# Performance work log

Hardware: AMD Instinct MI355X
Metric: run time of the kernel (lower is better)

Reference implementation:

```python
import jax, jax.numpy as jnp
import numpy as np

KH, KW = 3, 3      # kernel_size
SH, SW = 1, 1      # stride
MINVAL, MAXVAL = -0.45, -0.15


def setup_inputs() -> dict:
    key = jax.random.key(0)
    kx, kw = jax.random.split(key)
    x = jax.random.normal(kx, (16, 128, 128, 16), dtype=jnp.float32)  # NHWC
    W = jax.random.uniform(kw, (KH, KW, 16, 32), minval=MINVAL, maxval=MAXVAL,
                           dtype=jnp.float32)  # [kh, kw, C_in, filters]
    return {"x": x, "W": W}


def _dilation(x, W):
    # Max-plus sliding-window 'convolution' (VALID padding):
    # out[b,i,j,f] = max_{di,dj,c} x[b, i*SH+di, j*SW+dj, c] + W[di,dj,c,f]
    kh, kw, C, F = W.shape
    B, H, Wd, _ = x.shape
    Hout = (H - kh) // SH + 1
    Wout = (Wd - kw) // SW + 1
    out = jnp.full((B, Hout, Wout, F), -jnp.inf, dtype=x.dtype)
    for di in range(kh):          # small fixed loop over kernel offsets
        for dj in range(kw):
            xs = x[:, di:di + Hout * SH:SH, dj:dj + Wout * SW:SW, :]  # [B,Hout,Wout,C]
            # add W for this offset, reduce max over input channels
            out = jnp.maximum(out, jnp.max(xs[..., :, None] + W[di, dj], axis=3))
    return out


def reference(x, W):
    # erosion(x) = -dilation(-x)
    return -_dilation(-x, W)
```

## Files before the change

kernel.cpp:

```cpp
#include <hip/hip_runtime.h>
#include <math.h>


#define TI 42
#define TROWS (TI + 2)
#define LROW 64

typedef _Float16 h2 __attribute__((ext_vector_type(2)));

__device__ __forceinline__ h2 hmin2(h2 a, h2 b) {
    return __builtin_elementwise_min(a, b);
}

__device__ __forceinline__ h2 pkrtz(float a, float b) {
    auto r = __builtin_amdgcn_cvt_pkrtz(a, b);
    return *reinterpret_cast<h2*>(&r);
}

__device__ __forceinline__ h2 rowmin(const h2* hx, const h2 w[3][4]) {
    h2 t[12];
#pragma unroll
    for (int dj = 0; dj < 3; ++dj)
#pragma unroll
        for (int q = 0; q < 4; ++q)
            t[dj * 4 + q] = hx[dj * 4 + q] - w[dj][q];
#pragma unroll
    for (int k = 0; k < 6; ++k) t[k] = hmin2(t[k], t[k + 6]);
    t[0] = hmin2(t[0], t[3]);
    t[1] = hmin2(t[1], t[4]);
    t[2] = hmin2(t[2], t[5]);
    return hmin2(hmin2(t[0], t[1]), t[2]);
}

__global__ __launch_bounds__(256) void erosion_kernel(
    const float* __restrict__ x, const float* __restrict__ Wt,
    float* __restrict__ out)
{
    __shared__ _Float16 lds[2 * TROWS * LROW];

    const int tid = threadIdx.x;
    const int f  = tid & 31;
    const int ch = (tid >> 5) & 1;
    const int jt = tid >> 6;
    const int b  = blockIdx.z;
    const int i0 = blockIdx.y * TI;
    const int jb = blockIdx.x * 4;
    const int j  = jb + jt;
    const bool writer = (j < 126) && (ch == 0);

    {
        const float* xg = x + (size_t)b * (128 * 128 * 16);
        for (int t = tid; t < TROWS * 12; t += 256) {
            int r   = t / 12;
            int k   = t % 12;
            int cc  = k >> 1;
            int ch2 = k & 1;
            int col = min(jb + cc, 127);
            const float* src = xg + ((size_t)(i0 + r) * 128 + col) * 16 + ch2 * 8;
            float4 lo = *reinterpret_cast<const float4*>(src);
            float4 hi = *reinterpret_cast<const float4*>(src + 4);
            h2 o[4] = { pkrtz(lo.x, lo.y), pkrtz(lo.z, lo.w),
                        pkrtz(hi.x, hi.y), pkrtz(hi.z, hi.w) };
            *reinterpret_cast<float4*>(
                &lds[ch2 * (TROWS * LROW) + r * LROW + cc * 8]) =
                *reinterpret_cast<float4*>(o);
        }
    }

    h2 wh[3][3][4];
#pragma unroll
    for (int di = 0; di < 3; ++di)
#pragma unroll
        for (int dj = 0; dj < 3; ++dj)
#pragma unroll
            for (int q = 0; q < 4; ++q) {
                int p = di * 3 + dj;
                float a = Wt[(p * 16 + ch * 8 + 2 * q) * 32 + f];
                float c = Wt[(p * 16 + ch * 8 + 2 * q + 1) * 32 + f];
                wh[di][dj][q] = pkrtz(a, c);
            }

    __syncthreads();

    const _Float16* lb = &lds[ch * (TROWS * LROW) + jt * 8];
    float* op = out + (((size_t)b * 126 + i0) * 126 + j) * 32 + f;

    const _Float16 HINF = (_Float16)__builtin_huge_valf();
    h2 accB = {HINF, HINF};
    h2 accC = {HINF, HINF};

    auto body = [&](int r, bool do_store) {
        h2 hx[12];
#pragma unroll
        for (int dj = 0; dj < 3; ++dj) {
            float4 raw = *reinterpret_cast<const float4*>(lb + r * LROW + dj * 8);
            const h2* p = reinterpret_cast<const h2*>(&raw);
            hx[dj * 4 + 0] = p[0];
            hx[dj * 4 + 1] = p[1];
            hx[dj * 4 + 2] = p[2];
            hx[dj * 4 + 3] = p[3];
        }

        h2 n0 = rowmin(hx, wh[0]);
        h2 n1 = rowmin(hx, wh[1]);
        h2 n2 = rowmin(hx, wh[2]);

        h2 fin2 = hmin2(accC, n2);
        accC = hmin2(accB, n1);
        accB = n0;

        if (do_store) {
            _Float16 vm = fin2[0] < fin2[1] ? fin2[0] : fin2[1];
            float v = (float)vm;
            v = fminf(v, __shfl_xor(v, 32));
            if (writer)
                op[(size_t)(r - 2) * (126 * 32)] = v;
        }
    };

    body(0, false);
    body(1, false);
#pragma unroll 3
    for (int r = 2; r < TROWS; ++r)
        body(r, true);
}

extern "C" void kernel_launch(void* const* d_in, const int* in_sizes, int n_in,
                              void* d_out, int out_size, void* d_ws, size_t ws_size,
                              hipStream_t stream) {
    const float* x  = (const float*)d_in[0];
    const float* Wt = (const float*)d_in[1];
    float* out = (float*)d_out;

    dim3 grid(32, 3, 16);
    dim3 block(256);
    erosion_kernel<<<grid, block, 0, stream>>>(x, Wt, out);
}
```

Before: 113.6 us.

## Give each thread all 16 input channels and drop the cross-lane shuffle

The channel split across two half-waves goes away. Each thread now reduces over all 16 channels with 72 packed weights held in registers, so the __shfl_xor combine is no longer needed. The block covers 8 output columns instead of 4, the row tile shrinks from 42 to 21, and the grid changes to 16x6x16 while the block count stays the same. LDS becomes a single interleaved buffer with 16 channels per column. In exchange, register pressure roughly doubles for weights and inputs, and the halo row overhead grows because of the shorter row tiles.

```diff
diff --git a/kernel.cpp b/kernel.cpp
--- a/kernel.cpp
+++ b/kernel.cpp
@@ -2,9 +2,10 @@
 #include <math.h>
 
 
-#define TI 42
+#define TI 21
 #define TROWS (TI + 2)
-#define LROW 64
+#define TCOLS 10
+#define CROW (TCOLS * 16)
 
 typedef _Float16 h2 __attribute__((ext_vector_type(2)));
 
@@ -17,72 +18,53 @@
     return *reinterpret_cast<h2*>(&r);
 }
 
-__device__ __forceinline__ h2 rowmin(const h2* hx, const h2 w[3][4]) {
-    h2 t[12];
-#pragma unroll
-    for (int dj = 0; dj < 3; ++dj)
-#pragma unroll
-        for (int q = 0; q < 4; ++q)
-            t[dj * 4 + q] = hx[dj * 4 + q] - w[dj][q];
-#pragma unroll
-    for (int k = 0; k < 6; ++k) t[k] = hmin2(t[k], t[k + 6]);
-    t[0] = hmin2(t[0], t[3]);
-    t[1] = hmin2(t[1], t[4]);
-    t[2] = hmin2(t[2], t[5]);
-    return hmin2(hmin2(t[0], t[1]), t[2]);
-}
-
 __global__ __launch_bounds__(256) void erosion_kernel(
     const float* __restrict__ x, const float* __restrict__ Wt,
     float* __restrict__ out)
 {
-    __shared__ _Float16 lds[2 * TROWS * LROW];
+    __shared__ _Float16 lds[TROWS * CROW];
 
     const int tid = threadIdx.x;
     const int f  = tid & 31;
-    const int ch = (tid >> 5) & 1;
-    const int jt = tid >> 6;
+    const int jt = tid >> 5;
     const int b  = blockIdx.z;
     const int i0 = blockIdx.y * TI;
-    const int jb = blockIdx.x * 4;
+    const int jb = blockIdx.x * 8;
     const int j  = jb + jt;
-    const bool writer = (j < 126) && (ch == 0);
+    const bool writer = (j < 126);
 
     {
         const float* xg = x + (size_t)b * (128 * 128 * 16);
-        for (int t = tid; t < TROWS * 12; t += 256) {
-            int r   = t / 12;
-            int k   = t % 12;
-            int cc  = k >> 1;
-            int ch2 = k & 1;
+        for (int t = tid; t < TROWS * 40; t += 256) {
+            int r   = t / 40;
+            int k   = t % 40;
+            int cc  = k >> 2;
+            int q4  = k & 3;
             int col = min(jb + cc, 127);
-            const float* src = xg + ((size_t)(i0 + r) * 128 + col) * 16 + ch2 * 8;
-            float4 lo = *reinterpret_cast<const float4*>(src);
-            float4 hi = *reinterpret_cast<const float4*>(src + 4);
-            h2 o[4] = { pkrtz(lo.x, lo.y), pkrtz(lo.z, lo.w),
-                        pkrtz(hi.x, hi.y), pkrtz(hi.z, hi.w) };
-            *reinterpret_cast<float4*>(
-                &lds[ch2 * (TROWS * LROW) + r * LROW + cc * 8]) =
-                *reinterpret_cast<float4*>(o);
+            const float* src = xg + ((size_t)(i0 + r) * 128 + col) * 16 + q4 * 4;
+            float4 v = *reinterpret_cast<const float4*>(src);
+            h2 o[2] = { pkrtz(v.x, v.y), pkrtz(v.z, v.w) };
+            *reinterpret_cast<double*>(&lds[r * CROW + cc * 16 + q4 * 4]) =
+                *reinterpret_cast<double*>(o);
         }
     }
 
-    h2 wh[3][3][4];
+    h2 wh[3][3][8];
 #pragma unroll
     for (int di = 0; di < 3; ++di)
 #pragma unroll
         for (int dj = 0; dj < 3; ++dj)
 #pragma unroll
-            for (int q = 0; q < 4; ++q) {
+            for (int q = 0; q < 8; ++q) {
                 int p = di * 3 + dj;
-                float a = Wt[(p * 16 + ch * 8 + 2 * q) * 32 + f];
-                float c = Wt[(p * 16 + ch * 8 + 2 * q + 1) * 32 + f];
+                float a = Wt[(p * 16 + 2 * q) * 32 + f];
+                float c = Wt[(p * 16 + 2 * q + 1) * 32 + f];
                 wh[di][dj][q] = pkrtz(a, c);
             }
 
     __syncthreads();
 
-    const _Float16* lb = &lds[ch * (TROWS * LROW) + jt * 8];
+    const _Float16* lb = &lds[jt * 16];
     float* op = out + (((size_t)b * 126 + i0) * 126 + j) * 32 + f;
 
     const _Float16 HINF = (_Float16)__builtin_huge_valf();
@@ -90,31 +72,44 @@
     h2 accC = {HINF, HINF};
 
     auto body = [&](int r, bool do_store) {
-        h2 hx[12];
+        h2 hx[3][8];
 #pragma unroll
         for (int dj = 0; dj < 3; ++dj) {
-            float4 raw = *reinterpret_cast<const float4*>(lb + r * LROW + dj * 8);
-            const h2* p = reinterpret_cast<const h2*>(&raw);
-            hx[dj * 4 + 0] = p[0];
-            hx[dj * 4 + 1] = p[1];
-            hx[dj * 4 + 2] = p[2];
-            hx[dj * 4 + 3] = p[3];
+            float4 lo = *reinterpret_cast<const float4*>(lb + r * CROW + dj * 16);
+            float4 hi = *reinterpret_cast<const float4*>(lb + r * CROW + dj * 16 + 8);
+            const h2* pl = reinterpret_cast<const h2*>(&lo);
+            const h2* ph = reinterpret_cast<const h2*>(&hi);
+#pragma unroll
+            for (int q = 0; q < 4; ++q) { hx[dj][q] = pl[q]; hx[dj][4 + q] = ph[q]; }
         }
 
-        h2 n0 = rowmin(hx, wh[0]);
-        h2 n1 = rowmin(hx, wh[1]);
-        h2 n2 = rowmin(hx, wh[2]);
+        h2 n[3];
+#pragma unroll
+        for (int di = 0; di < 3; ++di) {
+            h2 t[24];
+#pragma unroll
+            for (int dj = 0; dj < 3; ++dj)
+#pragma unroll
+                for (int q = 0; q < 8; ++q)
+                    t[dj * 8 + q] = hx[dj][q] - wh[di][dj][q];
+#pragma unroll
+            for (int k = 0; k < 12; ++k) t[k] = hmin2(t[k], t[k + 12]);
+#pragma unroll
+            for (int k = 0; k < 6; ++k)  t[k] = hmin2(t[k], t[k + 6]);
+#pragma unroll
+            for (int k = 0; k < 3; ++k)  t[k] = hmin2(t[k], t[k + 3]);
+            n[di] = hmin2(hmin2(t[0], t[1]), t[2]);
+        }
 
-        h2 fin2 = hmin2(accC, n2);
-        accC = hmin2(accB, n1);
-        accB = n0;
+        h2 fin2 = hmin2(accC, n[2]);
+        accC = hmin2(accB, n[1]);
+        accB = n[0];
 
         if (do_store) {
-            _Float16 vm = fin2[0] < fin2[1] ? fin2[0] : fin2[1];
-            float v = (float)vm;
-            v = fminf(v, __shfl_xor(v, 32));
+            _Float16 a = fin2[0], c = fin2[1];
+            _Float16 vm = a < c ? a : c;
             if (writer)
-                op[(size_t)(r - 2) * (126 * 32)] = v;
+                op[(size_t)(r - 2) * (126 * 32)] = (float)vm;
         }
     };
 
@@ -132,7 +127,7 @@
     const float* Wt = (const float*)d_in[1];
     float* out = (float*)d_out;
 
-    dim3 grid(32, 3, 16);
+    dim3 grid(16, 6, 16);
     dim3 block(256);
     erosion_kernel<<<grid, block, 0, stream>>>(x, Wt, out);
 }
```

Measured after the change: 137.6 us. 1.21x slower.

## Halve row tile, stage results in LDS, and prefetch next row into registers

Applied to the files above, without the earlier changes.

Each block now covers half as many output rows, and the grid doubles in the row dimension so more blocks are in flight. Per-row results are no longer reduced with a cross-lane shuffle and written straight to global memory. Each thread instead writes its half-channel minimum to a shared buffer, and after a barrier the block does one pass that combines the two channel halves and stores to global memory. The compute loop also loads the next input row from LDS into registers while the current row is being processed. The extra shared buffer (~13 KB) and the second barrier may reduce occupancy, and halving the tile increases the halo reload overhead.

```diff
diff --git a/kernel.cpp b/kernel.cpp
--- a/kernel.cpp
+++ b/kernel.cpp
@@ -2,9 +2,10 @@
 #include <math.h>
 
 
-#define TI 42
+#define TI 21
 #define TROWS (TI + 2)
 #define LROW 64
+#define VMS 26
 
 typedef _Float16 h2 __attribute__((ext_vector_type(2)));
 
@@ -36,7 +37,8 @@
     const float* __restrict__ x, const float* __restrict__ Wt,
     float* __restrict__ out)
 {
-    __shared__ _Float16 lds[2 * TROWS * LROW];
+    __shared__ _Float16 tile[2 * TROWS * LROW];
+    __shared__ _Float16 vmbuf[256 * VMS];
 
     const int tid = threadIdx.x;
     const int f  = tid & 31;
@@ -45,25 +47,27 @@
     const int b  = blockIdx.z;
     const int i0 = blockIdx.y * TI;
     const int jb = blockIdx.x * 4;
-    const int j  = jb + jt;
-    const bool writer = (j < 126) && (ch == 0);
 
     {
         const float* xg = x + (size_t)b * (128 * 128 * 16);
-        for (int t = tid; t < TROWS * 12; t += 256) {
-            int r   = t / 12;
-            int k   = t % 12;
-            int cc  = k >> 1;
-            int ch2 = k & 1;
-            int col = min(jb + cc, 127);
-            const float* src = xg + ((size_t)(i0 + r) * 128 + col) * 16 + ch2 * 8;
-            float4 lo = *reinterpret_cast<const float4*>(src);
-            float4 hi = *reinterpret_cast<const float4*>(src + 4);
-            h2 o[4] = { pkrtz(lo.x, lo.y), pkrtz(lo.z, lo.w),
-                        pkrtz(hi.x, hi.y), pkrtz(hi.z, hi.w) };
-            *reinterpret_cast<float4*>(
-                &lds[ch2 * (TROWS * LROW) + r * LROW + cc * 8]) =
-                *reinterpret_cast<float4*>(o);
+#pragma unroll
+        for (int pass = 0; pass < 2; ++pass) {
+            int t = tid + pass * 256;
+            if (t < TROWS * 12) {
+                int r   = t / 12;
+                int k   = t % 12;
+                int cc  = k >> 1;
+                int ch2 = k & 1;
+                int col = min(jb + cc, 127);
+                const float* src = xg + ((size_t)(i0 + r) * 128 + col) * 16 + ch2 * 8;
+                float4 lo = *reinterpret_cast<const float4*>(src);
+                float4 hi = *reinterpret_cast<const float4*>(src + 4);
+                h2 o[4] = { pkrtz(lo.x, lo.y), pkrtz(lo.z, lo.w),
+                            pkrtz(hi.x, hi.y), pkrtz(hi.z, hi.w) };
+                *reinterpret_cast<float4*>(
+                    &tile[ch2 * (TROWS * LROW) + r * LROW + cc * 8]) =
+                    *reinterpret_cast<float4*>(o);
+            }
         }
     }
 
@@ -82,23 +86,33 @@
 
     __syncthreads();
 
-    const _Float16* lb = &lds[ch * (TROWS * LROW) + jt * 8];
-    float* op = out + (((size_t)b * 126 + i0) * 126 + j) * 32 + f;
+    const _Float16* lb = &tile[ch * (TROWS * LROW) + jt * 8];
+    _Float16* vmp = &vmbuf[tid * VMS];
 
     const _Float16 HINF = (_Float16)__builtin_huge_valf();
     h2 accB = {HINF, HINF};
     h2 accC = {HINF, HINF};
 
-    auto body = [&](int r, bool do_store) {
+    float4 pre[3];
+#pragma unroll
+    for (int dj = 0; dj < 3; ++dj)
+        pre[dj] = *reinterpret_cast<const float4*>(lb + dj * 8);
+
+    auto body = [&](int r, bool do_prefetch, bool do_vm) {
         h2 hx[12];
 #pragma unroll
         for (int dj = 0; dj < 3; ++dj) {
-            float4 raw = *reinterpret_cast<const float4*>(lb + r * LROW + dj * 8);
-            const h2* p = reinterpret_cast<const h2*>(&raw);
+            const h2* p = reinterpret_cast<const h2*>(&pre[dj]);
             hx[dj * 4 + 0] = p[0];
             hx[dj * 4 + 1] = p[1];
             hx[dj * 4 + 2] = p[2];
             hx[dj * 4 + 3] = p[3];
+        }
+        if (do_prefetch) {
+            const _Float16* ln = lb + (r + 1) * LROW;
+#pragma unroll
+            for (int dj = 0; dj < 3; ++dj)
+                pre[dj] = *reinterpret_cast<const float4*>(ln + dj * 8);
         }
 
         h2 n0 = rowmin(hx, wh[0]);
@@ -109,20 +123,37 @@
         accC = hmin2(accB, n1);
         accB = n0;
 
-        if (do_store) {
-            _Float16 vm = fin2[0] < fin2[1] ? fin2[0] : fin2[1];
-            float v = (float)vm;
-            v = fminf(v, __shfl_xor(v, 32));
-            if (writer)
-                op[(size_t)(r - 2) * (126 * 32)] = v;
+        if (do_vm) {
+            _Float16 a = fin2[0], c = fin2[1];
+            _Float16 vm = a < c ? a : c;
+            vmp[r - 2] = vm;
         }
     };
 
-    body(0, false);
-    body(1, false);
+    body(0, true, false);
+    body(1, true, false);
 #pragma unroll 3
-    for (int r = 2; r < TROWS; ++r)
-        body(r, true);
+    for (int r = 2; r < TROWS - 1; ++r)
+        body(r, true, true);
+    body(TROWS - 1, false, true);
+
+    __syncthreads();
+
+    {
+        float* outb = out + (size_t)b * (126 * 126 * 32);
+        for (int t = tid; t < TI * 128; t += 256) {
+            int row = t >> 7;
+            int m   = t & 127;
+            int col = m >> 5;
+            int ff  = m & 31;
+            int jj  = jb + col;
+            _Float16 a = vmbuf[(col * 64 + ff) * VMS + row];
+            _Float16 c = vmbuf[(col * 64 + 32 + ff) * VMS + row];
+            _Float16 vm = a < c ? a : c;
+            if (jj < 126)
+                outb[((size_t)(i0 + row) * 126 + jj) * 32 + ff] = (float)vm;
+        }
+    }
 }
 
 extern "C" void kernel_launch(void* const* d_in, const int* in_sizes, int n_in,
@@ -132,7 +163,7 @@
     const float* Wt = (const float*)d_in[1];
     float* out = (float*)d_out;
 
-    dim3 grid(32, 3, 16);
+    dim3 grid(32, 6, 16);
     dim3 block(256);
     erosion_kernel<<<grid, block, 0, stream>>>(x, Wt, out);
 }
```

Measured after the change: 109.8 us. 1.03x faster.
